# Performance work log

Hardware: AMD Instinct MI355X
Metric: run time of the kernel (lower is better)

The kernel has to match this reference:

```python
import jax, jax.numpy as jnp
import numpy as np

B, S, D, H = 4, 2048, 1024, 16
DK = D // H
INFTY = 1000000.0
INIT_SCALE = 1.2  # RandomUniform(-1.2, 1.2) kernel initializer


def setup_inputs() -> dict:
    key = jax.random.key(0)
    ks = jax.random.split(key, 6)
    x = jax.random.normal(ks[0], (B, S, D), dtype=jnp.float32)
    mask = jax.random.randint(ks[1], (B, S), 0, 2) == 1  # bool padding mask
    WQ = jax.random.uniform(ks[2], (D, D), jnp.float32, -INIT_SCALE, INIT_SCALE)
    WK = jax.random.uniform(ks[3], (D, D), jnp.float32, -INIT_SCALE, INIT_SCALE)
    WV = jax.random.uniform(ks[4], (D, D), jnp.float32, -INIT_SCALE, INIT_SCALE)
    WO = jax.random.uniform(ks[5], (D, D), jnp.float32, -INIT_SCALE, INIT_SCALE)
    return {"x": x, "mask": mask, "WQ": WQ, "WK": WK, "WV": WV, "WO": WO}


def reference(x, mask, WQ, WK, WV, WO):
    # Faithful reproduction of the layout: reshape to (B, S, d_key, n_heads)
    # then permute, matching K.reshape/K.permute_dimensions in the original.
    q = (x @ WQ).reshape(B, S, DK, H).transpose(0, 3, 1, 2)  # (B, H, S, DK)
    k = (x @ WK).reshape(B, S, DK, H).transpose(0, 3, 2, 1)  # (B, H, DK, S)
    score = jnp.matmul(q, k) / np.sqrt(DK)                   # (B, H, S, S)
    # additive key masking: score - (~mask)[B,1,1,S] * infinity
    inv_mask = (~mask).astype(x.dtype)
    score = score - inv_mask[:, None, None, :] * INFTY
    score = jax.nn.softmax(score, axis=-1)                   # att_dropout == 0
    v = (x @ WV).reshape(B, S, DK, H).transpose(0, 3, 1, 2)  # (B, H, S, DK)
    o = jnp.matmul(score, v)                                 # (B, H, S, DK)
    o = o.transpose(0, 2, 1, 3).reshape(B, S, H * DK)
    o = o @ WO                                               # (B, S, D)
    # final query-position masking + abs, as in the original
    o = jnp.abs(o * mask.astype(x.dtype)[:, :, None])
    return o
```

## Files before the change

kernel.cpp:

```cpp
#include <hip/hip_runtime.h>
#include <hip/hip_bf16.h>
#include <cstdint>
#include <cstddef>

constexpr int Bc  = 4;
constexpr int Sc  = 2048;
constexpr int Dc  = 1024;
constexpr int Hc  = 16;
constexpr int DKc = 64;
constexpr int Mtot = Bc * Sc;
constexpr float SC2  = 0.125f * 1.4426950408889634f;
constexpr float INF2 = 1000000.0f * 1.4426950408889634f;
constexpr float SXq  = 5400.0f;
constexpr float SWq  = 27166.0f;
constexpr float INVS = 1.0f / (SXq * SWq);

typedef short bf16x8 __attribute__((ext_vector_type(8)));
typedef float f32x4  __attribute__((ext_vector_type(4)));
typedef int   i32x4  __attribute__((ext_vector_type(4)));
typedef unsigned int u32x4 __attribute__((ext_vector_type(4)));

__device__ inline unsigned short bf16_rn(float f) {
    uint32_t u = __float_as_uint(f);
    uint32_t r = (u + 0x7FFFu + ((u >> 16) & 1u)) >> 16;
    return (unsigned short)r;
}
__device__ inline uint32_t pk_bf16(float a, float b) {
    uint32_t d;
    asm("v_cvt_pk_bf16_f32 %0, %1, %2" : "=v"(d) : "v"(a), "v"(b));
    return d;
}
__device__ inline int perm64(int k) {
    return (k & ~63) | (((k & 15) << 2) | ((k >> 4) & 3));
}
__device__ inline void mfma_i8(i32x4& acc, u32x4 a, u32x4 b) {
    asm volatile("v_mfma_i32_16x16x64_i8 %0, %1, %2, %0" : "+v"(acc) : "v"(a), "v"(b));
}
__device__ inline void split_i16(int fx, char& h, char& l) {
    int lo = ((fx + 128) & 255) - 128;
    h = (char)((fx - lo) >> 8);
    l = (char)lo;
}
__device__ inline void gl_lds16(const void* g, void* l) {
    __builtin_amdgcn_global_load_lds(
        (const __attribute__((address_space(1))) unsigned int*)g,
        (__attribute__((address_space(3))) unsigned int*)l, 16, 0, 0);
}

__global__ __launch_bounds__(256) void mask_norm(const void* __restrict__ mraw,
                                                 int* __restrict__ rinv,
                                                 int* __restrict__ nbv,
                                                 int* __restrict__ npadv) {
    __shared__ int fF32, fU8, fI32;
    __shared__ int part[256];
    __shared__ int nb_sh;
    if (threadIdx.x == 0) { fF32 = 0; fU8 = 0; fI32 = 0; }
    __syncthreads();
    const unsigned char* mb = (const unsigned char*)mraw;
    int aF = 0, a1 = 0, a4 = 0;
    for (int i = threadIdx.x; i < Mtot; i += 256) {
        unsigned char v = mb[i];
        if ((i & 3) == 3 && v == 0x3F) aF = 1;
        if (v) {
            if (i & 3) a1 = 1;
            else if (i & 7) a4 = 1;
        }
    }
    if (aF) fF32 = 1;
    if (a1) fU8 = 1;
    if (a4) fI32 = 1;
    __syncthreads();

    const int b = blockIdx.x;
    const int sbase = b * Sc + threadIdx.x * 8;
    int loc[8], cnt = 0;
    if (fF32) {
        const float* mf = (const float*)mraw;
        #pragma unroll
        for (int u = 0; u < 8; ++u) { loc[u] = (mf[sbase + u] != 0.0f); cnt += loc[u]; }
    } else if (fU8) {
        #pragma unroll
        for (int u = 0; u < 8; ++u) { loc[u] = (mb[sbase + u] != 0); cnt += loc[u]; }
    } else if (fI32) {
        const int* m32 = (const int*)mraw;
        #pragma unroll
        for (int u = 0; u < 8; ++u) { loc[u] = (m32[sbase + u] != 0); cnt += loc[u]; }
    } else {
        const long long* m64 = (const long long*)mraw;
        #pragma unroll
        for (int u = 0; u < 8; ++u) { loc[u] = (m64[sbase + u] != 0); cnt += loc[u]; }
    }
    part[threadIdx.x] = cnt;
    __syncthreads();
    if (threadIdx.x == 0) {
        int run = 0;
        for (int i = 0; i < 256; ++i) { int c = part[i]; part[i] = run; run += c; }
        nbv[b] = run;
        npadv[b] = (run + 63) & ~63;
        nb_sh = run;
    }
    __syncthreads();
    const int nbb = nb_sh;
    int pos = part[threadIdx.x];
    #pragma unroll
    for (int u = 0; u < 8; ++u) {
        const int s = threadIdx.x * 8 + u;
        if (loc[u]) {
            rinv[b * Sc + pos] = s;
            pos++;
        } else {
            rinv[b * Sc + nbb + (s - pos)] = s;
        }
    }
}

__global__ __launch_bounds__(256) void quant_x(const float* __restrict__ x,
                                               unsigned short* __restrict__ xhi,
                                               signed char* __restrict__ xh8,
                                               signed char* __restrict__ xl8) {
    const int i = (blockIdx.x * 256 + threadIdx.x) * 4;
    float4 v = *reinterpret_cast<const float4*>(x + i);
    ushort4 hb;
    hb.x = bf16_rn(v.x); hb.y = bf16_rn(v.y); hb.z = bf16_rn(v.z); hb.w = bf16_rn(v.w);
    *reinterpret_cast<ushort4*>(xhi + i) = hb;
    char4 h8, l8;
    int fx;
    fx = min(max(__float2int_rn(v.x * SXq), -32640), 32640); split_i16(fx, h8.x, l8.x);
    fx = min(max(__float2int_rn(v.y * SXq), -32640), 32640); split_i16(fx, h8.y, l8.y);
    fx = min(max(__float2int_rn(v.z * SXq), -32640), 32640); split_i16(fx, h8.z, l8.z);
    fx = min(max(__float2int_rn(v.w * SXq), -32640), 32640); split_i16(fx, h8.w, l8.w);
    *reinterpret_cast<char4*>(xh8 + i) = h8;
    *reinterpret_cast<char4*>(xl8 + i) = l8;
}

__global__ __launch_bounds__(256) void prep_w(
    const float* __restrict__ WQ, const float* __restrict__ WK,
    const float* __restrict__ WV, const float* __restrict__ WO,
    signed char* __restrict__ WQh8, signed char* __restrict__ WQl8,
    signed char* __restrict__ WKh8, signed char* __restrict__ WKl8,
    unsigned short* __restrict__ WVh, unsigned short* __restrict__ WOh,
    const int* __restrict__ nbv, const int* __restrict__ npadv,
    unsigned short* __restrict__ Khi, unsigned short* __restrict__ Klo,
    unsigned short* __restrict__ Vt) {
    const int z = blockIdx.z;
    const int t = threadIdx.x;

    if (z == 4) {
        const int idx = blockIdx.y * 16 + blockIdx.x;
        const int bh = idx >> 2, prt = idx & 3;
        const int b = bh >> 4;
        const int nb = nbv[b], np = npadv[b];
        const size_t kbase = (size_t)bh * Sc * DKc;
        const size_t vbase = (size_t)bh * DKc * Sc;
        const int n = (np - nb) * DKc;
        for (int i = prt * 256 + t; i < n; i += 1024) {
            const int r = nb + i / DKc, c = i % DKc;
            Khi[kbase + (size_t)r * DKc + c] = 0;
            Klo[kbase + (size_t)r * DKc + c] = 0;
            Vt[vbase + (size_t)c * Sc + r] = 0;
        }
        return;
    }

    __shared__ float ls[64][68];
    const float* W = (z == 0) ? WQ : (z == 1) ? WK : (z == 2) ? WV : WO;
    const int k0 = blockIdx.y * 64, n0 = blockIdx.x * 64;
    #pragma unroll
    for (int l = 0; l < 4; ++l) {
        const int idx = t + l * 256;
        const int r = idx >> 4, c = (idx & 15) * 4;
        *reinterpret_cast<float4*>(&ls[r][c]) =
            *reinterpret_cast<const float4*>(W + (size_t)(k0 + r) * Dc + n0 + c);
    }
    __syncthreads();

    if (z <= 1) {
        signed char* Wh8 = z ? WKh8 : WQh8;
        signed char* Wl8 = z ? WKl8 : WQl8;
        #pragma unroll
        for (int l = 0; l < 4; ++l) {
            const int idx = t + l * 256;
            const int on = idx >> 4, kq = (idx & 15) * 4;
            char4 hv, lv;
            int fx;
            fx = __float2int_rn(ls[kq + 0][on] * SWq); split_i16(fx, hv.x, lv.x);
            fx = __float2int_rn(ls[kq + 1][on] * SWq); split_i16(fx, hv.y, lv.y);
            fx = __float2int_rn(ls[kq + 2][on] * SWq); split_i16(fx, hv.z, lv.z);
            fx = __float2int_rn(ls[kq + 3][on] * SWq); split_i16(fx, hv.w, lv.w);
            const size_t o = (size_t)(n0 + on) * Dc + k0 + kq;
            *reinterpret_cast<char4*>(Wh8 + o) = hv;
            *reinterpret_cast<char4*>(Wl8 + o) = lv;
        }
    } else {
        unsigned short* Wh = (z == 2) ? WVh : WOh;
        const bool PERM = (z == 3);
        #pragma unroll
        for (int l = 0; l < 4; ++l) {
            const int idx = t + l * 256;
            const int on = idx >> 4, kq = (idx & 15) * 4;
            #pragma unroll
            for (int j = 0; j < 4; ++j) {
                const float v = ls[kq + j][on];
                const int k  = k0 + kq + j;
                const int kd = PERM ? perm64(k) : k;
                Wh[(size_t)(n0 + on) * Dc + kd] = bf16_rn(v);
            }
        }
    }
}

__global__ __launch_bounds__(256) void gemm_qkv(
    const signed char* __restrict__ xh8, const signed char* __restrict__ xl8,
    const unsigned short* __restrict__ xhi,
    const signed char* __restrict__ WQh8, const signed char* __restrict__ WQl8,
    const signed char* __restrict__ WKh8, const signed char* __restrict__ WKl8,
    const unsigned short* __restrict__ WVh,
    const int* __restrict__ rinv, const int* __restrict__ nbv,
    unsigned short* __restrict__ Qhi, unsigned short* __restrict__ Qlo,
    unsigned short* __restrict__ Khi, unsigned short* __restrict__ Klo,
    unsigned short* __restrict__ Vt) {
    __shared__ __align__(16) char S[24576];
    const int z = blockIdx.z;
    const int t = threadIdx.x;
    const int n0 = blockIdx.x * 128;
    const int wv = t >> 6, lane = t & 63, li = lane & 15, lg = lane >> 4;

    if (z < 2) {
        const int m0 = blockIdx.y * 64;
        const int b = m0 >> 11, mm0 = m0 & 2047;
        const int nb = nbv[b];
        if (mm0 >= nb) return;
        const int wm = (wv >> 1) * 32, wn = (wv & 1) * 64;

        signed char* Ah = (signed char*)S;
        signed char* Al = (signed char*)S + 4096;
        signed char* Bh = (signed char*)S + 8192;
        signed char* Bl = (signed char*)S + 16384;
        const signed char* Bh8 = z ? WKh8 : WQh8;
        const signed char* Bl8 = z ? WKl8 : WQl8;
        const float scale = z ? INVS : (SC2 * INVS);
        unsigned short* O1 = z ? Khi : Qhi;
        unsigned short* O2 = z ? Klo : Qlo;

        const int arow = wv * 16 + (lane >> 2);
        const size_t gAr = ((size_t)b * Sc + rinv[b * Sc + mm0 + arow]) * Dc;
        int rowN[2];
        #pragma unroll
        for (int c = 0; c < 2; ++c) rowN[c] = n0 + (wv * 2 + c) * 16 + (lane >> 2);
        const int cq = (lane & 3) * 16;

        i32x4 a1[2][4] = {};
        i32x4 a2[2][4] = {};
        asm volatile("s_nop 7" :::);

        for (int k0 = 0; k0 < Dc; k0 += 64) {
            __syncthreads();
            gl_lds16(xh8 + gAr + k0 + cq, &Ah[wv * 1024]);
            gl_lds16(xl8 + gAr + k0 + cq, &Al[wv * 1024]);
            #pragma unroll
            for (int c = 0; c < 2; ++c) {
                const int ci = wv * 2 + c;
                const size_t gb = (size_t)rowN[c] * Dc + k0 + cq;
                gl_lds16(Bh8 + gb, &Bh[ci * 1024]);
                gl_lds16(Bl8 + gb, &Bl[ci * 1024]);
            }
            __syncthreads();

            u32x4 bhf[4], blf[4];
            #pragma unroll
            for (int ni = 0; ni < 4; ++ni) {
                bhf[ni] = *reinterpret_cast<const u32x4*>(&Bh[(wn + ni * 16 + li) * 64 + lg * 16]);
                blf[ni] = *reinterpret_cast<const u32x4*>(&Bl[(wn + ni * 16 + li) * 64 + lg * 16]);
            }
            #pragma unroll
            for (int mi = 0; mi < 2; ++mi) {
                const u32x4 ahf = *reinterpret_cast<const u32x4*>(&Ah[(wm + mi * 16 + li) * 64 + lg * 16]);
                const u32x4 alf = *reinterpret_cast<const u32x4*>(&Al[(wm + mi * 16 + li) * 64 + lg * 16]);
                #pragma unroll
                for (int ni = 0; ni < 4; ++ni) {
                    mfma_i8(a1[mi][ni], ahf, bhf[ni]);
                    mfma_i8(a2[mi][ni], ahf, blf[ni]);
                    mfma_i8(a2[mi][ni], alf, bhf[ni]);
                }
            }
        }

        asm volatile("s_nop 7\ns_nop 7\ns_nop 7" :::);

        const int dkb = (n0 + wn) >> 4;
        #pragma unroll
        for (int mi = 0; mi < 2; ++mi) {
            #pragma unroll
            for (int r = 0; r < 4; ++r) {
                const int cs = mm0 + wm + mi * 16 + lg * 4 + r;
                if (cs >= nb) continue;
                const size_t ob = ((size_t)(b * Hc + li) * Sc + cs) * DKc + dkb;
                ushort4 hq, lq;
                float fv[4];
                #pragma unroll
                for (int ni = 0; ni < 4; ++ni)
                    fv[ni] = fmaf((float)a1[mi][ni][r], 65536.0f,
                                  (float)a2[mi][ni][r] * 256.0f) * scale;
                hq.x = bf16_rn(fv[0]); hq.y = bf16_rn(fv[1]);
                hq.z = bf16_rn(fv[2]); hq.w = bf16_rn(fv[3]);
                lq.x = bf16_rn(fv[0] - __uint_as_float((uint32_t)hq.x << 16));
                lq.y = bf16_rn(fv[1] - __uint_as_float((uint32_t)hq.y << 16));
                lq.z = bf16_rn(fv[2] - __uint_as_float((uint32_t)hq.z << 16));
                lq.w = bf16_rn(fv[3] - __uint_as_float((uint32_t)hq.w << 16));
                *reinterpret_cast<ushort4*>(O1 + ob) = hq;
                *reinterpret_cast<ushort4*>(O2 + ob) = lq;
            }
        }
    } else {
        if (blockIdx.y >= 64) return;
        const int m0 = blockIdx.y * 128;
        const int b = m0 >> 11, mm0 = m0 & 2047;
        const int nb = nbv[b];
        if (mm0 >= nb) return;
        const int wm = (wv >> 1) * 64, wn = (wv & 1) * 64;

        unsigned short* Ah = (unsigned short*)S;
        unsigned short* Bh = (unsigned short*)(S + 8192);

        size_t gAr[2];
        int rowN[2];
        #pragma unroll
        for (int c = 0; c < 2; ++c) {
            const int ci  = wv * 2 + c;
            const int row = ci * 16 + (lane >> 2);
            rowN[c] = n0 + row;
            gAr[c] = ((size_t)b * Sc + rinv[b * Sc + mm0 + row]) * Dc;
        }
        const int cq = (lane & 3) * 8;

        f32x4 acc[4][4] = {};

        for (int k0 = 0; k0 < Dc; k0 += 32) {
            __syncthreads();
            #pragma unroll
            for (int c = 0; c < 2; ++c) {
                const int ci = wv * 2 + c;
                gl_lds16(xhi + gAr[c] + k0 + cq, &Ah[ci * 512]);
                gl_lds16(WVh + (size_t)rowN[c] * Dc + k0 + cq, &Bh[ci * 512]);
            }
            __syncthreads();

            bf16x8 bhf[4];
            #pragma unroll
            for (int ni = 0; ni < 4; ++ni)
                bhf[ni] = *reinterpret_cast<const bf16x8*>(&Bh[(wn + ni * 16 + li) * 32 + lg * 8]);
            #pragma unroll
            for (int mi = 0; mi < 4; ++mi) {
                const bf16x8 ahf = *reinterpret_cast<const bf16x8*>(&Ah[(wm + mi * 16 + li) * 32 + lg * 8]);
                #pragma unroll
                for (int ni = 0; ni < 4; ++ni)
                    acc[mi][ni] = __builtin_amdgcn_mfma_f32_16x16x32_bf16(ahf, bhf[ni], acc[mi][ni], 0, 0, 0);
            }
        }

        #pragma unroll
        for (int mi = 0; mi < 4; ++mi) {
            const int csb = mm0 + wm + mi * 16 + lg * 4;
            #pragma unroll
            for (int ni = 0; ni < 4; ++ni) {
                const int n = n0 + wn + ni * 16 + li;
                const int h = n & 15, dk = n >> 4;
                const size_t ob = ((size_t)(b * Hc + h) * DKc + dk) * Sc + csb;
                if (csb + 3 < nb) {
                    ushort4 vq;
                    vq.x = bf16_rn(acc[mi][ni][0]);
                    vq.y = bf16_rn(acc[mi][ni][1]);
                    vq.z = bf16_rn(acc[mi][ni][2]);
                    vq.w = bf16_rn(acc[mi][ni][3]);
                    *reinterpret_cast<ushort4*>(Vt + ob) = vq;
                } else {
                    #pragma unroll
                    for (int r = 0; r < 4; ++r)
                        if (csb + r < nb) Vt[ob + r] = bf16_rn(acc[mi][ni][r]);
                }
            }
        }
    }
}

__global__ __launch_bounds__(256) void gemm_oproj(
    const unsigned short* __restrict__ Ahi,
    const unsigned short* __restrict__ Bhi,
    const int* __restrict__ rinv, const int* __restrict__ nbv,
    float* __restrict__ Of) {
    __shared__ __align__(16) unsigned short Ah[128 * 32];
    __shared__ __align__(16) unsigned short Bh[128 * 32];
    const int t = threadIdx.x;
    const int n0 = blockIdx.x * 128, m0 = blockIdx.y * 128;
    const int b = m0 >> 11, mm0 = m0 & 2047;
    const int nb = nbv[b];
    const int wv = t >> 6, lane = t & 63, li = lane & 15, lg = lane >> 4;
    const int wm = (wv >> 1) * 64, wn = (wv & 1) * 64;

    if (mm0 >= nb) {
        #pragma unroll
        for (int mi = 0; mi < 4; ++mi) {
            #pragma unroll
            for (int r = 0; r < 4; ++r) {
                const int cs = mm0 + wm + mi * 16 + lg * 4 + r;
                const int gs = rinv[b * Sc + cs];
                #pragma unroll
                for (int ni = 0; ni < 4; ++ni) {
                    const int n = n0 + wn + ni * 16 + li;
                    Of[((size_t)(b * Sc + gs)) * Dc + n] = 0.0f;
                }
            }
        }
        return;
    }

    f32x4 acc[4][4] = {};

    for (int k0 = 0; k0 < Dc; k0 += 32) {
        __syncthreads();
        #pragma unroll
        for (int c = 0; c < 2; ++c) {
            const int ci  = wv * 2 + c;
            const int row = ci * 16 + (lane >> 2);
            const int cq  = (lane & 3) * 8;
            gl_lds16(Ahi + (size_t)(m0 + row) * Dc + k0 + cq, &Ah[ci * 512]);
            gl_lds16(Bhi + (size_t)(n0 + row) * Dc + k0 + cq, &Bh[ci * 512]);
        }
        __syncthreads();

        bf16x8 bhf[4];
        #pragma unroll
        for (int ni = 0; ni < 4; ++ni)
            bhf[ni] = *reinterpret_cast<const bf16x8*>(&Bh[(wn + ni * 16 + li) * 32 + lg * 8]);
        #pragma unroll
        for (int mi = 0; mi < 4; ++mi) {
            const bf16x8 ahf = *reinterpret_cast<const bf16x8*>(&Ah[(wm + mi * 16 + li) * 32 + lg * 8]);
            #pragma unroll
            for (int ni = 0; ni < 4; ++ni)
                acc[mi][ni] = __builtin_amdgcn_mfma_f32_16x16x32_bf16(ahf, bhf[ni], acc[mi][ni], 0, 0, 0);
        }
    }

    #pragma unroll
    for (int mi = 0; mi < 4; ++mi) {
        #pragma unroll
        for (int r = 0; r < 4; ++r) {
            const int cs = mm0 + wm + mi * 16 + lg * 4 + r;
            const int gs = rinv[b * Sc + cs];
            const bool valid = (cs < nb);
            #pragma unroll
            for (int ni = 0; ni < 4; ++ni) {
                const int n = n0 + wn + ni * 16 + li;
                Of[((size_t)(b * Sc + gs)) * Dc + n] =
                    valid ? fabsf(acc[mi][ni][r]) : 0.0f;
            }
        }
    }
}

__global__ __launch_bounds__(512) void attn_mfma(const unsigned short* __restrict__ Qhi,
                                                 const unsigned short* __restrict__ Qlo,
                                                 const unsigned short* __restrict__ Khi,
                                                 const unsigned short* __restrict__ Klo,
                                                 const unsigned short* __restrict__ Vtg,
                                                 const int* __restrict__ nbv,
                                                 const int* __restrict__ npadv,
                                                 unsigned short* __restrict__ att) {
    constexpr int TK = 64;
    const int id  = blockIdx.x;
    const int swz = (id & 7) * 128 + (id >> 3);
    const int qb  = swz & 15;
    const int bh  = swz >> 4;
    const int b = bh >> 4, h = bh & 15;
    const int q0 = qb * 128;
    const int nb = nbv[b];
    if (q0 >= nb) return;
    const int ntile = npadv[b] >> 6;
    const int nt2 = (ntile + 1) >> 1;

    __shared__ __align__(16) unsigned short PsKs[2][128][72];
    __shared__ __align__(16) unsigned short Vs[2][80][72];

    const int t    = threadIdx.x;
    const int grp  = t >> 8;
    const int tg   = t & 255;
    const int wave = tg >> 6;
    const int lane = t & 63;
    const int lg   = lane >> 4;
    const int li   = lane & 15;

    const int myBase = grp ? nt2 : 0;
    const int myEnd  = grp ? ntile : nt2;

    {
        const int r = 64 + (tg >> 4), c4 = (tg & 15) * 4;
        const unsigned short val = ((tg >> 4) == 0) ? (unsigned short)0x3F80 : (unsigned short)0;
        ushort4 v; v.x = val; v.y = val; v.z = val; v.w = val;
        *reinterpret_cast<ushort4*>(&Vs[grp][r][c4]) = v;
    }

    bf16x8 qh[2][2], ql[2][2];
    #pragma unroll
    for (int hf = 0; hf < 2; ++hf) {
        const size_t qrow = ((size_t)bh * Sc + q0 + wave * 32 + hf * 16 + li) * DKc + lg * 8;
        qh[hf][0] = *reinterpret_cast<const bf16x8*>(Qhi + qrow);
        qh[hf][1] = *reinterpret_cast<const bf16x8*>(Qhi + qrow + 32);
        ql[hf][0] = *reinterpret_cast<const bf16x8*>(Qlo + qrow);
        ql[hf][1] = *reinterpret_cast<const bf16x8*>(Qlo + qrow + 32);
    }

    const size_t kbase = (size_t)bh * Sc * DKc;
    const size_t vbase = (size_t)bh * DKc * Sc;

    f32x4 accO[2][5] = {};
    float m[2][4];
    #pragma unroll
    for (int hf = 0; hf < 2; ++hf)
        #pragma unroll
        for (int r = 0; r < 4; ++r) m[hf][r] = -1e30f;

    for (int it = 0; it < nt2; ++it) {
        const int kt = myBase + it;
        const bool act = (kt < myEnd);
        const int k0 = kt * TK;
        __syncthreads();
        if (act) {
            #pragma unroll
            for (int u = 0; u < 2; ++u) {
                const int idx = tg + u * 256;
                const int r = idx >> 3, cc = (idx & 7) * 8;
                *reinterpret_cast<uint4*>(&PsKs[grp][r][cc]) =
                    *reinterpret_cast<const uint4*>(Khi + kbase + (size_t)(k0 + r) * DKc + cc);
                *reinterpret_cast<uint4*>(&PsKs[grp][64 + r][cc]) =
                    *reinterpret_cast<const uint4*>(Klo + kbase + (size_t)(k0 + r) * DKc + cc);
                *reinterpret_cast<uint4*>(&Vs[grp][r][cc]) =
                    *reinterpret_cast<const uint4*>(Vtg + vbase + (size_t)r * Sc + k0 + cc);
            }
        }
        __syncthreads();
        if (!act) continue;

        float sc[2][4][4];
        #pragma unroll
        for (int n = 0; n < 4; ++n) {
            const bf16x8 kh0 = *reinterpret_cast<const bf16x8*>(&PsKs[grp][n * 16 + li][lg * 8]);
            const bf16x8 kh1 = *reinterpret_cast<const bf16x8*>(&PsKs[grp][n * 16 + li][32 + lg * 8]);
            const bf16x8 kl0 = *reinterpret_cast<const bf16x8*>(&PsKs[grp][64 + n * 16 + li][lg * 8]);
            const bf16x8 kl1 = *reinterpret_cast<const bf16x8*>(&PsKs[grp][64 + n * 16 + li][32 + lg * 8]);
            const float mz = (k0 + n * 16 + li < nb) ? 0.0f : INF2;
            #pragma unroll
            for (int hf = 0; hf < 2; ++hf) {
                f32x4 a = {0, 0, 0, 0};
                a = __builtin_amdgcn_mfma_f32_16x16x32_bf16(qh[hf][0], kh0, a, 0, 0, 0);
                a = __builtin_amdgcn_mfma_f32_16x16x32_bf16(qh[hf][1], kh1, a, 0, 0, 0);
                a = __builtin_amdgcn_mfma_f32_16x16x32_bf16(qh[hf][0], kl0, a, 0, 0, 0);
                a = __builtin_amdgcn_mfma_f32_16x16x32_bf16(qh[hf][1], kl1, a, 0, 0, 0);
                a = __builtin_amdgcn_mfma_f32_16x16x32_bf16(ql[hf][0], kh0, a, 0, 0, 0);
                a = __builtin_amdgcn_mfma_f32_16x16x32_bf16(ql[hf][1], kh1, a, 0, 0, 0);
                #pragma unroll
                for (int r = 0; r < 4; ++r) sc[hf][n][r] = a[r] - mz;
            }
        }

        float mx[2][4], rs[2][4];
        #pragma unroll
        for (int hf = 0; hf < 2; ++hf)
            #pragma unroll
            for (int r = 0; r < 4; ++r)
                mx[hf][r] = fmaxf(fmaxf(sc[hf][0][r], sc[hf][1][r]),
                                  fmaxf(sc[hf][2][r], sc[hf][3][r]));
        #pragma unroll
        for (int o = 1; o < 16; o <<= 1)
            #pragma unroll
            for (int hf = 0; hf < 2; ++hf)
                #pragma unroll
                for (int r = 0; r < 4; ++r)
                    mx[hf][r] = fmaxf(mx[hf][r], __shfl_xor(mx[hf][r], o));
        #pragma unroll
        for (int hf = 0; hf < 2; ++hf)
            #pragma unroll
            for (int r = 0; r < 4; ++r) {
                const float mn = fmaxf(m[hf][r], mx[hf][r]);
                rs[hf][r] = exp2f(m[hf][r] - mn);
                m[hf][r]  = mn;
            }
        #pragma unroll
        for (int hf = 0; hf < 2; ++hf)
            #pragma unroll
            for (int r = 0; r < 4; ++r) {
                const int row = wave * 32 + hf * 16 + lg * 4 + r;
                const uint32_t w01 = pk_bf16(exp2f(sc[hf][0][r] - m[hf][r]),
                                             exp2f(sc[hf][1][r] - m[hf][r]));
                const uint32_t w23 = pk_bf16(exp2f(sc[hf][2][r] - m[hf][r]),
                                             exp2f(sc[hf][3][r] - m[hf][r]));
                PsKs[grp][row][li]      = (unsigned short)w01;
                PsKs[grp][row][li + 16] = (unsigned short)(w01 >> 16);
                PsKs[grp][row][li + 32] = (unsigned short)w23;
                PsKs[grp][row][li + 48] = (unsigned short)(w23 >> 16);
            }

        #pragma unroll
        for (int hf = 0; hf < 2; ++hf)
            #pragma unroll
            for (int dt = 0; dt < 5; ++dt)
                #pragma unroll
                for (int r = 0; r < 4; ++r)
                    accO[hf][dt][r] *= rs[hf][r];

        #pragma unroll
        for (int c = 0; c < 2; ++c) {
            bf16x8 pa[2];
            #pragma unroll
            for (int hf = 0; hf < 2; ++hf)
                pa[hf] = *reinterpret_cast<const bf16x8*>(&PsKs[grp][wave * 32 + hf * 16 + li][c * 32 + lg * 8]);
            #pragma unroll
            for (int dt = 0; dt < 5; ++dt) {
                const bf16x8 vb = *reinterpret_cast<const bf16x8*>(&Vs[grp][dt * 16 + li][c * 32 + lg * 8]);
                #pragma unroll
                for (int hf = 0; hf < 2; ++hf)
                    accO[hf][dt] = __builtin_amdgcn_mfma_f32_16x16x32_bf16(pa[hf], vb, accO[hf][dt], 0, 0, 0);
            }
        }
    }

    __syncthreads();
    float* pO  = (float*)&PsKs[0][0][0];
    float* pML = pO + 128 * 64;

    if (grp == 1) {
        #pragma unroll
        for (int hf = 0; hf < 2; ++hf) {
            #pragma unroll
            for (int r = 0; r < 4; ++r) {
                const int row = wave * 32 + hf * 16 + lg * 4 + r;
                if (li == 0) {
                    pML[row * 2]     = m[hf][r];
                    pML[row * 2 + 1] = accO[hf][4][r];
                }
                float4 o = make_float4(accO[hf][0][r], accO[hf][1][r],
                                       accO[hf][2][r], accO[hf][3][r]);
                *reinterpret_cast<float4*>(&pO[row * 64 + li * 4]) = o;
            }
        }
    }
    __syncthreads();
    if (grp == 0) {
        #pragma unroll
        for (int hf = 0; hf < 2; ++hf) {
            #pragma unroll
            for (int r = 0; r < 4; ++r) {
                const int row = wave * 32 + hf * 16 + lg * 4 + r;
                const float m1 = pML[row * 2];
                const float l1 = pML[row * 2 + 1];
                const float l0 = __shfl(accO[hf][4][r], lane & 0x30);
                const float ms = fmaxf(m[hf][r], m1);
                const float s0 = exp2f(m[hf][r] - ms);
                const float s1 = exp2f(m1 - ms);
                const float inv = 1.0f / (l0 * s0 + l1 * s1);
                const float4 o1 = *reinterpret_cast<const float4*>(&pO[row * 64 + li * 4]);
                const int q = q0 + row;
                uint2 w;
                w.x = pk_bf16((accO[hf][0][r] * s0 + o1.x * s1) * inv,
                              (accO[hf][1][r] * s0 + o1.y * s1) * inv);
                w.y = pk_bf16((accO[hf][2][r] * s0 + o1.z * s1) * inv,
                              (accO[hf][3][r] * s0 + o1.w * s1) * inv);
                *reinterpret_cast<uint2*>(att + (size_t)(b * Sc + q) * Dc + h * DKc + li * 4) = w;
            }
        }
    }
}

extern "C" void kernel_launch(void* const* d_in, const int* in_sizes, int n_in,
                              void* d_out, int out_size, void* d_ws, size_t ws_size,
                              hipStream_t stream) {
    const float* x    = (const float*)d_in[0];
    const void*  mraw = d_in[1];
    const float* WQ   = (const float*)d_in[2];
    const float* WK   = (const float*)d_in[3];
    const float* WV   = (const float*)d_in[4];
    const float* WO   = (const float*)d_in[5];
    float* out = (float*)d_out;

    int* rinv  = (int*)d_ws;
    int* nbv   = rinv + Mtot;
    int* npadv = nbv + 4;
    const size_t SZ = (size_t)Mtot * Dc;
    const size_t WSZ = (size_t)Dc * Dc;
    char* p = (char*)d_ws + 65664;
    unsigned short* xhi = (unsigned short*)p;            p += SZ * 2;
    signed char*    xh8 = (signed char*)p;               p += SZ;
    signed char*    xl8 = (signed char*)p;               p += SZ;
    unsigned short* WVh = (unsigned short*)p;            p += WSZ * 2;
    unsigned short* WOh = (unsigned short*)p;            p += WSZ * 2;
    signed char*    WQh8 = (signed char*)p;              p += WSZ;
    signed char*    WQl8 = (signed char*)p;              p += WSZ;
    signed char*    WKh8 = (signed char*)p;              p += WSZ;
    signed char*    WKl8 = (signed char*)p;              p += WSZ;
    unsigned short* Qhi = (unsigned short*)p;            p += SZ * 2;
    unsigned short* Qlo = (unsigned short*)p;            p += SZ * 2;
    unsigned short* Khi = (unsigned short*)p;            p += SZ * 2;
    unsigned short* Klo = (unsigned short*)p;            p += SZ * 2;
    unsigned short* Vt  = (unsigned short*)p;            p += SZ * 2;
    unsigned short* att = xhi;

    mask_norm<<<dim3(4), 256, 0, stream>>>(mraw, rinv, nbv, npadv);
    quant_x<<<(int)(SZ / 1024), 256, 0, stream>>>(x, xhi, xh8, xl8);
    prep_w<<<dim3(16, 16, 5), 256, 0, stream>>>(WQ, WK, WV, WO,
                                                WQh8, WQl8, WKh8, WKl8,
                                                WVh, WOh, nbv, npadv,
                                                Khi, Klo, Vt);

    gemm_qkv<<<dim3(8, 128, 3), 256, 0, stream>>>(xh8, xl8, xhi,
                                                  WQh8, WQl8, WKh8, WKl8, WVh,
                                                  rinv, nbv,
                                                  Qhi, Qlo, Khi, Klo, Vt);

    attn_mfma<<<dim3(1024), 512, 0, stream>>>(Qhi, Qlo, Khi, Klo, Vt, nbv, npadv, att);

    gemm_oproj<<<dim3(8, 64), 256, 0, stream>>>(att, WOh, rinv, nbv, out);
}
```

Before: 262.1 us.

## Compute V projection with split int8 MFMA and shrink O-proj tile rows

The V projection now uses the same split-int8 (hi/lo) MFMA path as Q and K instead of a separate bf16 GEMM branch. This lets quant_x drop the bf16 copy of x and lets prep_w emit int8 hi/lo V weights. The attention output buffer now aliases the int8 x buffers. Separately, the output projection tile shrinks from 128 to 64 rows, doubling the grid. The V path does three int8 MFMAs per step in place of one bf16 MFMA, which costs compute but saves x memory traffic and the bf16 conversion. The smaller O-proj tile gives more blocks at lower per-block reuse.

```diff
diff --git a/kernel.cpp b/kernel.cpp
--- a/kernel.cpp
+++ b/kernel.cpp
@@ -115,14 +115,10 @@
 }
 
 __global__ __launch_bounds__(256) void quant_x(const float* __restrict__ x,
-                                               unsigned short* __restrict__ xhi,
                                                signed char* __restrict__ xh8,
                                                signed char* __restrict__ xl8) {
     const int i = (blockIdx.x * 256 + threadIdx.x) * 4;
     float4 v = *reinterpret_cast<const float4*>(x + i);
-    ushort4 hb;
-    hb.x = bf16_rn(v.x); hb.y = bf16_rn(v.y); hb.z = bf16_rn(v.z); hb.w = bf16_rn(v.w);
-    *reinterpret_cast<ushort4*>(xhi + i) = hb;
     char4 h8, l8;
     int fx;
     fx = min(max(__float2int_rn(v.x * SXq), -32640), 32640); split_i16(fx, h8.x, l8.x);
@@ -138,7 +134,8 @@
     const float* __restrict__ WV, const float* __restrict__ WO,
     signed char* __restrict__ WQh8, signed char* __restrict__ WQl8,
     signed char* __restrict__ WKh8, signed char* __restrict__ WKl8,
-    unsigned short* __restrict__ WVh, unsigned short* __restrict__ WOh,
+    signed char* __restrict__ WVh8, signed char* __restrict__ WVl8,
+    unsigned short* __restrict__ WOh,
     const int* __restrict__ nbv, const int* __restrict__ npadv,
     unsigned short* __restrict__ Khi, unsigned short* __restrict__ Klo,
     unsigned short* __restrict__ Vt) {
@@ -174,9 +171,9 @@
     }
     __syncthreads();
 
-    if (z <= 1) {
-        signed char* Wh8 = z ? WKh8 : WQh8;
-        signed char* Wl8 = z ? WKl8 : WQl8;
+    if (z <= 2) {
+        signed char* Wh8 = (z == 0) ? WQh8 : (z == 1) ? WKh8 : WVh8;
+        signed char* Wl8 = (z == 0) ? WQl8 : (z == 1) ? WKl8 : WVl8;
         #pragma unroll
         for (int l = 0; l < 4; ++l) {
             const int idx = t + l * 256;
@@ -192,8 +189,6 @@
             *reinterpret_cast<char4*>(Wl8 + o) = lv;
         }
     } else {
-        unsigned short* Wh = (z == 2) ? WVh : WOh;
-        const bool PERM = (z == 3);
         #pragma unroll
         for (int l = 0; l < 4; ++l) {
             const int idx = t + l * 256;
@@ -201,9 +196,8 @@
             #pragma unroll
             for (int j = 0; j < 4; ++j) {
                 const float v = ls[kq + j][on];
-                const int k  = k0 + kq + j;
-                const int kd = PERM ? perm64(k) : k;
-                Wh[(size_t)(n0 + on) * Dc + kd] = bf16_rn(v);
+                const int kd = perm64(k0 + kq + j);
+                WOh[(size_t)(n0 + on) * Dc + kd] = bf16_rn(v);
             }
         }
     }
@@ -211,10 +205,9 @@
 
 __global__ __launch_bounds__(256) void gemm_qkv(
     const signed char* __restrict__ xh8, const signed char* __restrict__ xl8,
-    const unsigned short* __restrict__ xhi,
     const signed char* __restrict__ WQh8, const signed char* __restrict__ WQl8,
     const signed char* __restrict__ WKh8, const signed char* __restrict__ WKl8,
-    const unsigned short* __restrict__ WVh,
+    const signed char* __restrict__ WVh8, const signed char* __restrict__ WVl8,
     const int* __restrict__ rinv, const int* __restrict__ nbv,
     unsigned short* __restrict__ Qhi, unsigned short* __restrict__ Qlo,
     unsigned short* __restrict__ Khi, unsigned short* __restrict__ Klo,
@@ -223,71 +216,70 @@
     const int z = blockIdx.z;
     const int t = threadIdx.x;
     const int n0 = blockIdx.x * 128;
+    const int m0 = blockIdx.y * 64;
+    const int b = m0 >> 11, mm0 = m0 & 2047;
+    const int nb = nbv[b];
+    if (mm0 >= nb) return;
     const int wv = t >> 6, lane = t & 63, li = lane & 15, lg = lane >> 4;
-
+    const int wm = (wv >> 1) * 32, wn = (wv & 1) * 64;
+
+    signed char* Ah = (signed char*)S;
+    signed char* Al = (signed char*)S + 4096;
+    signed char* Bh = (signed char*)S + 8192;
+    signed char* Bl = (signed char*)S + 16384;
+    const signed char* Bh8 = (z == 0) ? WQh8 : (z == 1) ? WKh8 : WVh8;
+    const signed char* Bl8 = (z == 0) ? WQl8 : (z == 1) ? WKl8 : WVl8;
+    const float scale = (z == 0) ? (SC2 * INVS) : INVS;
+
+    const int arow = wv * 16 + (lane >> 2);
+    const size_t gAr = ((size_t)b * Sc + rinv[b * Sc + mm0 + arow]) * Dc;
+    int rowN[2];
+    #pragma unroll
+    for (int c = 0; c < 2; ++c) rowN[c] = n0 + (wv * 2 + c) * 16 + (lane >> 2);
+    const int cq = (lane & 3) * 16;
+
+    i32x4 a1[2][4] = {};
+    i32x4 a2[2][4] = {};
+    asm volatile("s_nop 7" :::);
+
+    for (int k0 = 0; k0 < Dc; k0 += 64) {
+        __syncthreads();
+        gl_lds16(xh8 + gAr + k0 + cq, &Ah[wv * 1024]);
+        gl_lds16(xl8 + gAr + k0 + cq, &Al[wv * 1024]);
+        #pragma unroll
+        for (int c = 0; c < 2; ++c) {
+            const int ci = wv * 2 + c;
+            const size_t gb = (size_t)rowN[c] * Dc + k0 + cq;
+            gl_lds16(Bh8 + gb, &Bh[ci * 1024]);
+            gl_lds16(Bl8 + gb, &Bl[ci * 1024]);
+        }
+        __syncthreads();
+
+        u32x4 bhf[4], blf[4];
+        #pragma unroll
+        for (int ni = 0; ni < 4; ++ni) {
+            bhf[ni] = *reinterpret_cast<const u32x4*>(&Bh[(wn + ni * 16 + li) * 64 + lg * 16]);
+            blf[ni] = *reinterpret_cast<const u32x4*>(&Bl[(wn + ni * 16 + li) * 64 + lg * 16]);
+        }
+        #pragma unroll
+        for (int mi = 0; mi < 2; ++mi) {
+            const u32x4 ahf = *reinterpret_cast<const u32x4*>(&Ah[(wm + mi * 16 + li) * 64 + lg * 16]);
+            const u32x4 alf = *reinterpret_cast<const u32x4*>(&Al[(wm + mi * 16 + li) * 64 + lg * 16]);
+            #pragma unroll
+            for (int ni = 0; ni < 4; ++ni) {
+                mfma_i8(a1[mi][ni], ahf, bhf[ni]);
+                mfma_i8(a2[mi][ni], ahf, blf[ni]);
+                mfma_i8(a2[mi][ni], alf, bhf[ni]);
+            }
+        }
+    }
+
+    asm volatile("s_nop 7\ns_nop 7\ns_nop 7" :::);
+
+    const int dkb = (n0 + wn) >> 4;
     if (z < 2) {
-        const int m0 = blockIdx.y * 64;
-        const int b = m0 >> 11, mm0 = m0 & 2047;
-        const int nb = nbv[b];
-        if (mm0 >= nb) return;
-        const int wm = (wv >> 1) * 32, wn = (wv & 1) * 64;
-
-        signed char* Ah = (signed char*)S;
-        signed char* Al = (signed char*)S + 4096;
-        signed char* Bh = (signed char*)S + 8192;
-        signed char* Bl = (signed char*)S + 16384;
-        const signed char* Bh8 = z ? WKh8 : WQh8;
-        const signed char* Bl8 = z ? WKl8 : WQl8;
-        const float scale = z ? INVS : (SC2 * INVS);
         unsigned short* O1 = z ? Khi : Qhi;
         unsigned short* O2 = z ? Klo : Qlo;
-
-        const int arow = wv * 16 + (lane >> 2);
-        const size_t gAr = ((size_t)b * Sc + rinv[b * Sc + mm0 + arow]) * Dc;
-        int rowN[2];
-        #pragma unroll
-        for (int c = 0; c < 2; ++c) rowN[c] = n0 + (wv * 2 + c) * 16 + (lane >> 2);
-        const int cq = (lane & 3) * 16;
-
-        i32x4 a1[2][4] = {};
-        i32x4 a2[2][4] = {};
-        asm volatile("s_nop 7" :::);
-
-        for (int k0 = 0; k0 < Dc; k0 += 64) {
-            __syncthreads();
-            gl_lds16(xh8 + gAr + k0 + cq, &Ah[wv * 1024]);
-            gl_lds16(xl8 + gAr + k0 + cq, &Al[wv * 1024]);
-            #pragma unroll
-            for (int c = 0; c < 2; ++c) {
-                const int ci = wv * 2 + c;
-                const size_t gb = (size_t)rowN[c] * Dc + k0 + cq;
-                gl_lds16(Bh8 + gb, &Bh[ci * 1024]);
-                gl_lds16(Bl8 + gb, &Bl[ci * 1024]);
-            }
-            __syncthreads();
-
-            u32x4 bhf[4], blf[4];
-            #pragma unroll
-            for (int ni = 0; ni < 4; ++ni) {
-                bhf[ni] = *reinterpret_cast<const u32x4*>(&Bh[(wn + ni * 16 + li) * 64 + lg * 16]);
-                blf[ni] = *reinterpret_cast<const u32x4*>(&Bl[(wn + ni * 16 + li) * 64 + lg * 16]);
-            }
-            #pragma unroll
-            for (int mi = 0; mi < 2; ++mi) {
-                const u32x4 ahf = *reinterpret_cast<const u32x4*>(&Ah[(wm + mi * 16 + li) * 64 + lg * 16]);
-                const u32x4 alf = *reinterpret_cast<const u32x4*>(&Al[(wm + mi * 16 + li) * 64 + lg * 16]);
-                #pragma unroll
-                for (int ni = 0; ni < 4; ++ni) {
-                    mfma_i8(a1[mi][ni], ahf, bhf[ni]);
-                    mfma_i8(a2[mi][ni], ahf, blf[ni]);
-                    mfma_i8(a2[mi][ni], alf, bhf[ni]);
-                }
-            }
-        }
-
-        asm volatile("s_nop 7\ns_nop 7\ns_nop 7" :::);
-
-        const int dkb = (n0 + wn) >> 4;
         #pragma unroll
         for (int mi = 0; mi < 2; ++mi) {
             #pragma unroll
@@ -312,71 +304,26 @@
             }
         }
     } else {
-        if (blockIdx.y >= 64) return;
-        const int m0 = blockIdx.y * 128;
-        const int b = m0 >> 11, mm0 = m0 & 2047;
-        const int nb = nbv[b];
-        if (mm0 >= nb) return;
-        const int wm = (wv >> 1) * 64, wn = (wv & 1) * 64;
-
-        unsigned short* Ah = (unsigned short*)S;
-        unsigned short* Bh = (unsigned short*)(S + 8192);
-
-        size_t gAr[2];
-        int rowN[2];
-        #pragma unroll
-        for (int c = 0; c < 2; ++c) {
-            const int ci  = wv * 2 + c;
-            const int row = ci * 16 + (lane >> 2);
-            rowN[c] = n0 + row;
-            gAr[c] = ((size_t)b * Sc + rinv[b * Sc + mm0 + row]) * Dc;
-        }
-        const int cq = (lane & 3) * 8;
-
-        f32x4 acc[4][4] = {};
-
-        for (int k0 = 0; k0 < Dc; k0 += 32) {
-            __syncthreads();
-            #pragma unroll
-            for (int c = 0; c < 2; ++c) {
-                const int ci = wv * 2 + c;
-                gl_lds16(xhi + gAr[c] + k0 + cq, &Ah[ci * 512]);
-                gl_lds16(WVh + (size_t)rowN[c] * Dc + k0 + cq, &Bh[ci * 512]);
-            }
-            __syncthreads();
-
-            bf16x8 bhf[4];
-            #pragma unroll
-            for (int ni = 0; ni < 4; ++ni)
-                bhf[ni] = *reinterpret_cast<const bf16x8*>(&Bh[(wn + ni * 16 + li) * 32 + lg * 8]);
-            #pragma unroll
-            for (int mi = 0; mi < 4; ++mi) {
-                const bf16x8 ahf = *reinterpret_cast<const bf16x8*>(&Ah[(wm + mi * 16 + li) * 32 + lg * 8]);
+        #pragma unroll
+        for (int mi = 0; mi < 2; ++mi) {
+            const int csb = mm0 + wm + mi * 16 + lg * 4;
+            #pragma unroll
+            for (int ni = 0; ni < 4; ++ni) {
+                const size_t ob = ((size_t)(b * Hc + li) * DKc + dkb + ni) * Sc + csb;
+                float fv[4];
                 #pragma unroll
-                for (int ni = 0; ni < 4; ++ni)
-                    acc[mi][ni] = __builtin_amdgcn_mfma_f32_16x16x32_bf16(ahf, bhf[ni], acc[mi][ni], 0, 0, 0);
-            }
-        }
-
-        #pragma unroll
-        for (int mi = 0; mi < 4; ++mi) {
-            const int csb = mm0 + wm + mi * 16 + lg * 4;
-            #pragma unroll
-            for (int ni = 0; ni < 4; ++ni) {
-                const int n = n0 + wn + ni * 16 + li;
-                const int h = n & 15, dk = n >> 4;
-                const size_t ob = ((size_t)(b * Hc + h) * DKc + dk) * Sc + csb;
+                for (int r = 0; r < 4; ++r)
+                    fv[r] = fmaf((float)a1[mi][ni][r], 65536.0f,
+                                 (float)a2[mi][ni][r] * 256.0f) * INVS;
                 if (csb + 3 < nb) {
                     ushort4 vq;
-                    vq.x = bf16_rn(acc[mi][ni][0]);
-                    vq.y = bf16_rn(acc[mi][ni][1]);
-                    vq.z = bf16_rn(acc[mi][ni][2]);
-                    vq.w = bf16_rn(acc[mi][ni][3]);
+                    vq.x = bf16_rn(fv[0]); vq.y = bf16_rn(fv[1]);
+                    vq.z = bf16_rn(fv[2]); vq.w = bf16_rn(fv[3]);
                     *reinterpret_cast<ushort4*>(Vt + ob) = vq;
                 } else {
                     #pragma unroll
                     for (int r = 0; r < 4; ++r)
-                        if (csb + r < nb) Vt[ob + r] = bf16_rn(acc[mi][ni][r]);
+                        if (csb + r < nb) Vt[ob + r] = bf16_rn(fv[r]);
                 }
             }
         }
@@ -388,18 +335,18 @@
     const unsigned short* __restrict__ Bhi,
     const int* __restrict__ rinv, const int* __restrict__ nbv,
     float* __restrict__ Of) {
-    __shared__ __align__(16) unsigned short Ah[128 * 32];
+    __shared__ __align__(16) unsigned short Ah[64 * 32];
     __shared__ __align__(16) unsigned short Bh[128 * 32];
     const int t = threadIdx.x;
-    const int n0 = blockIdx.x * 128, m0 = blockIdx.y * 128;
+    const int n0 = blockIdx.x * 128, m0 = blockIdx.y * 64;
     const int b = m0 >> 11, mm0 = m0 & 2047;
     const int nb = nbv[b];
     const int wv = t >> 6, lane = t & 63, li = lane & 15, lg = lane >> 4;
-    const int wm = (wv >> 1) * 64, wn = (wv & 1) * 64;
+    const int wm = (wv >> 1) * 32, wn = (wv & 1) * 64;
 
     if (mm0 >= nb) {
         #pragma unroll
-        for (int mi = 0; mi < 4; ++mi) {
+        for (int mi = 0; mi < 2; ++mi) {
             #pragma unroll
             for (int r = 0; r < 4; ++r) {
                 const int cs = mm0 + wm + mi * 16 + lg * 4 + r;
@@ -414,17 +361,21 @@
         return;
     }
 
-    f32x4 acc[4][4] = {};
+    const int arow = wv * 16 + (lane >> 2);
+    const int acq = (lane & 3) * 8;
+    int rowN[2];
+    #pragma unroll
+    for (int c = 0; c < 2; ++c) rowN[c] = n0 + (wv * 2 + c) * 16 + (lane >> 2);
+
+    f32x4 acc[2][4] = {};
 
     for (int k0 = 0; k0 < Dc; k0 += 32) {
         __syncthreads();
+        gl_lds16(Ahi + (size_t)(m0 + arow) * Dc + k0 + acq, &Ah[wv * 512]);
         #pragma unroll
         for (int c = 0; c < 2; ++c) {
-            const int ci  = wv * 2 + c;
-            const int row = ci * 16 + (lane >> 2);
-            const int cq  = (lane & 3) * 8;
-            gl_lds16(Ahi + (size_t)(m0 + row) * Dc + k0 + cq, &Ah[ci * 512]);
-            gl_lds16(Bhi + (size_t)(n0 + row) * Dc + k0 + cq, &Bh[ci * 512]);
+            const int ci = wv * 2 + c;
+            gl_lds16(Bhi + (size_t)rowN[c] * Dc + k0 + acq, &Bh[ci * 512]);
         }
         __syncthreads();
 
@@ -433,7 +384,7 @@
         for (int ni = 0; ni < 4; ++ni)
             bhf[ni] = *reinterpret_cast<const bf16x8*>(&Bh[(wn + ni * 16 + li) * 32 + lg * 8]);
         #pragma unroll
-        for (int mi = 0; mi < 4; ++mi) {
+        for (int mi = 0; mi < 2; ++mi) {
             const bf16x8 ahf = *reinterpret_cast<const bf16x8*>(&Ah[(wm + mi * 16 + li) * 32 + lg * 8]);
             #pragma unroll
             for (int ni = 0; ni < 4; ++ni)
@@ -442,7 +393,7 @@
     }
 
     #pragma unroll
-    for (int mi = 0; mi < 4; ++mi) {
+    for (int mi = 0; mi < 2; ++mi) {
         #pragma unroll
         for (int r = 0; r < 4; ++r) {
             const int cs = mm0 + wm + mi * 16 + lg * 4 + r;
@@ -687,35 +638,36 @@
     const size_t SZ = (size_t)Mtot * Dc;
     const size_t WSZ = (size_t)Dc * Dc;
     char* p = (char*)d_ws + 65664;
-    unsigned short* xhi = (unsigned short*)p;            p += SZ * 2;
     signed char*    xh8 = (signed char*)p;               p += SZ;
     signed char*    xl8 = (signed char*)p;               p += SZ;
-    unsigned short* WVh = (unsigned short*)p;            p += WSZ * 2;
     unsigned short* WOh = (unsigned short*)p;            p += WSZ * 2;
     signed char*    WQh8 = (signed char*)p;              p += WSZ;
     signed char*    WQl8 = (signed char*)p;              p += WSZ;
     signed char*    WKh8 = (signed char*)p;              p += WSZ;
     signed char*    WKl8 = (signed char*)p;              p += WSZ;
+    signed char*    WVh8 = (signed char*)p;              p += WSZ;
+    signed char*    WVl8 = (signed char*)p;              p += WSZ;
     unsigned short* Qhi = (unsigned short*)p;            p += SZ * 2;
     unsigned short* Qlo = (unsigned short*)p;            p += SZ * 2;
     unsigned short* Khi = (unsigned short*)p;            p += SZ * 2;
     unsigned short* Klo = (unsigned short*)p;            p += SZ * 2;
     unsigned short* Vt  = (unsigned short*)p;            p += SZ * 2;
-    unsigned short* att = xhi;
+    unsigned short* att = (unsigned short*)xh8;
 
     mask_norm<<<dim3(4), 256, 0, stream>>>(mraw, rinv, nbv, npadv);
-    quant_x<<<(int)(SZ / 1024), 256, 0, stream>>>(x, xhi, xh8, xl8);
+    quant_x<<<(int)(SZ / 1024), 256, 0, stream>>>(x, xh8, xl8);
     prep_w<<<dim3(16, 16, 5), 256, 0, stream>>>(WQ, WK, WV, WO,
                                                 WQh8, WQl8, WKh8, WKl8,
-                                                WVh, WOh, nbv, npadv,
+                                                WVh8, WVl8, WOh, nbv, npadv,
                                                 Khi, Klo, Vt);
 
-    gemm_qkv<<<dim3(8, 128, 3), 256, 0, stream>>>(xh8, xl8, xhi,
-                                                  WQh8, WQl8, WKh8, WKl8, WVh,
+    gemm_qkv<<<dim3(8, 128, 3), 256, 0, stream>>>(xh8, xl8,
+                                                  WQh8, WQl8, WKh8, WKl8,
+                                                  WVh8, WVl8,
                                                   rinv, nbv,
                                                   Qhi, Qlo, Khi, Klo, Vt);
 
     attn_mfma<<<dim3(1024), 512, 0, stream>>>(Qhi, Qlo, Khi, Klo, Vt, nbv, npadv, att);
 
-    gemm_oproj<<<dim3(8, 64), 256, 0, stream>>>(att, WOh, rinv, nbv, out);
-}
+    gemm_oproj<<<dim3(8, 128), 256, 0, stream>>>(att, WOh, rinv, nbv, out);
+}
```

Result: faster. 252.7 us, median of 2 (-3.6%).
